# Kernel tuning notes

Hardware: AMD Instinct MI355X
Metric: run time of the kernel (lower is better)

The kernel has to match this reference:

```python
import jax, jax.numpy as jnp
import numpy as np

NUM_USERS = 4096
NUM_ITEMS = 4096
NUM_CLASSES = 5
INPUT_DIM = 64
H0 = 64   # hidden[0]
H1 = 32   # hidden[1]
BU = 2048
BV = 2048


def setup_inputs() -> dict:
    key = jax.random.key(0)
    ks = jax.random.split(key, 9)
    ridx = jax.random.randint(ks[0], (NUM_USERS, NUM_ITEMS), 0, NUM_CLASSES * 10)
    ratings = (jnp.arange(NUM_CLASSES)[:, None, None] == ridx[None]).astype(jnp.float32)
    u = jax.random.randint(ks[1], (BU,), 0, NUM_USERS)
    v = jax.random.randint(ks[2], (BV,), 0, NUM_ITEMS)
    u_emb = jax.random.normal(ks[3], (NUM_USERS, INPUT_DIM), jnp.float32) * 0.1
    v_emb = jax.random.normal(ks[4], (NUM_ITEMS, INPUT_DIM), jnp.float32) * 0.1
    gc_w = jax.random.normal(ks[5], (NUM_CLASSES, INPUT_DIM, H0), jnp.float32) / np.sqrt(INPUT_DIM)
    gc_b = jnp.zeros((NUM_CLASSES, H0), jnp.float32)
    dense_w = jax.random.normal(ks[6], (H0, H1), jnp.float32) / np.sqrt(H0)
    dense_b = jnp.zeros((H1,), jnp.float32)
    dec_w = jax.random.normal(ks[7], (NUM_CLASSES, H1, H1), jnp.float32) / np.sqrt(H1)
    return dict(u=u, v=v, ratings=ratings, u_emb=u_emb, v_emb=v_emb,
                gc_w=gc_w, gc_b=gc_b, dense_w=dense_w, dense_b=dense_b, dec_w=dec_w)


def reference(u, v, ratings, u_emb, v_emb, gc_w, gc_b, dense_w, dense_b, dec_w):
    bu = u.shape[0]
    # m = index_select(index_select(ratings, 1, u), 2, v)  -> [C, bu, bv]
    m = ratings[:, u][:, :, v]
    ue = u_emb[u]                      # [bu, D]
    ve = v_emb[v]                      # [bv, D]
    # Degree normalization exactly as in the torch code:
    # du = |sum over dim1 then dim0| -> per-item counts [bv]; di -> per-user counts [bu]
    du = jnp.abs(jnp.sum(m, axis=(0, 1)))
    di = jnp.abs(jnp.sum(m, axis=(0, 2)))
    c = jnp.concatenate([du, di])      # [bv + bu] (requires bu == bv, as in original)
    c = jnp.where(c > 0, 1.0 / c, 0.0)
    x = jnp.concatenate([ue, ve], axis=0)              # [bu+bv, D]
    # Per-class graph convolution, summed over rating classes.
    support = jnp.einsum('nd,cdh->cnh', x, gc_w)       # [C, N, H0]
    su, sv = support[:, :bu], support[:, bu:]
    agg_u = jnp.einsum('cuv,cvh->cuh', m, sv)          # users aggregate items
    agg_v = jnp.einsum('cuv,cuh->cvh', m, su)          # items aggregate users
    agg = jnp.concatenate([agg_u, agg_v], axis=1)      # [C, N, H0]
    z = jnp.sum(c[None, :, None] * agg + gc_b[:, None, :], axis=0)
    z = jax.nn.relu(z)
    hidden = jax.nn.sigmoid(z @ dense_w + dense_b)     # [N, H1]
    hu, hv = hidden[:bu], hidden[bu:]
    # Bilinear decoder: per-class logits u^T W_c v  -> [C, bu, bv]
    logits = jnp.einsum('ud,cde,ve->cuv', hu, dec_w, hv)
    probs = jax.nn.softmax(logits, axis=0)
    classes = jnp.arange(NUM_CLASSES, dtype=hidden.dtype)
    m_hat = jnp.einsum('c,cuv->uv', classes, probs)    # expected rating
    observed = jnp.sum(m, axis=0)                      # [bu, bv] in {0,1}
    n_obs = jnp.maximum(jnp.sum(observed), 1.0)
    logp = jax.nn.log_softmax(logits, axis=0)
    loss = -jnp.sum(m * logp) / n_obs
    pred = jnp.argmax(logits, axis=0)
    true = jnp.argmax(m, axis=0)
    accuracy = jnp.sum((pred == true) * observed) / n_obs
    return m_hat, loss, accuracy
```

## Files before the change

### kernel.cpp

```cpp
#include <hip/hip_runtime.h>
#include <hip/hip_bf16.h>
#include <cstdint>

#define RST 16777216
typedef unsigned short u16;
typedef unsigned char u8;
typedef __attribute__((ext_vector_type(8))) short short8v;
typedef __attribute__((ext_vector_type(4))) float f32x4;

__device__ __forceinline__ u16 f2bf(float x){
  unsigned int b = __float_as_uint(x);
  unsigned int r = (b + 0x7FFFu + ((b >> 16) & 1u)) >> 16;
  return (u16)r;
}
__device__ __forceinline__ float bf2f(u16 h){
  return __uint_as_float(((unsigned int)h) << 16);
}
__device__ __forceinline__ void split8(const float* fa, short8v& hi, short8v& lo){
#pragma unroll
  for (int e = 0; e < 8; e++){
    u16 h = f2bf(fa[e]);
    hi[e] = (short)h;
    lo[e] = (short)f2bf(fa[e] - bf2f(h));
  }
}

__global__ __launch_bounds__(256) void k_labels(const int* __restrict__ u, const int* __restrict__ v,
                                                const float* __restrict__ ratings, u8* __restrict__ L,
                                                int* __restrict__ di){
  __shared__ float row[4096];
  __shared__ int wsum[4];
  int i = blockIdx.x;
  int tid = threadIdx.x;
  int lane = tid & 63, wid = tid >> 6;
  int U = u[i];
  int j0 = tid * 8;
  int vj[8];
#pragma unroll
  for (int k = 0; k < 8; k++) vj[k] = v[j0 + k];
  int lab[8];
#pragma unroll
  for (int k = 0; k < 8; k++) lab[k] = 5;
  const float* rbase = ratings + (size_t)U * 4096;
  for (int c = 0; c < 5; c++){
    const float4* src = (const float4*)(rbase + (size_t)c * RST);
#pragma unroll
    for (int k = 0; k < 4; k++) ((float4*)row)[tid + k*256] = src[tid + k*256];
    __syncthreads();
#pragma unroll
    for (int k = 0; k < 8; k++) if (row[vj[k]] > 0.5f) lab[k] = c;
    __syncthreads();
  }
  unsigned int lo = 0, hi = 0;
  int cnt = 0;
#pragma unroll
  for (int k = 0; k < 4; k++){
    lo |= ((unsigned)lab[k]) << (8*k); hi |= ((unsigned)lab[k+4]) << (8*k);
    cnt += (lab[k] != 5); cnt += (lab[k+4] != 5);
  }
  *(uint2*)(L + (size_t)i * 2048 + j0) = make_uint2(lo, hi);
#pragma unroll
  for (int o = 32; o > 0; o >>= 1) cnt += __shfl_down(cnt, o);
  if (lane == 0) wsum[wid] = cnt;
  __syncthreads();
  if (tid == 0) di[i] = wsum[0] + wsum[1] + wsum[2] + wsum[3];
}

__global__ __launch_bounds__(256) void k_trsup(const u8* __restrict__ L, u8* __restrict__ LT,
    const int* __restrict__ u, const int* __restrict__ v,
    const float* __restrict__ u_emb, const float* __restrict__ v_emb, const float* __restrict__ gc_w,
    float* __restrict__ S){
  __shared__ u8 tile[64][64];
  int tid = threadIdx.x;
  if (blockIdx.x < 1024){
    int jb = blockIdx.x & 31, ib = blockIdx.x >> 5;
    int i0 = ib * 64, j0 = jb * 64;
    int r = tid >> 2, cq = tid & 3;
    uint4 d = *(const uint4*)(L + (size_t)(i0 + r) * 2048 + j0 + cq * 16);
    *(uint4*)&tile[r][cq * 16] = d;
    __syncthreads();
    u8 ob[16];
#pragma unroll
    for (int k = 0; k < 16; k++) ob[k] = tile[cq * 16 + k][r];
    *(uint4*)(LT + (size_t)(j0 + r) * 2048 + i0 + cq * 16) = *(uint4*)ob;
  } else {
    int b = blockIdx.x - 1024;
    int c = b >> 6, nblk = b & 63;
    int lane = tid & 63, wv = tid >> 6;
    int m = lane & 15, q = lane >> 4;
    int n0 = nblk * 64;
    bool uside = (n0 < 2048);
    const int* nidx = uside ? u : v;
    const float* emb = uside ? u_emb : v_emb;
    int nbase = uside ? n0 : (n0 - 2048);
    int h0 = wv * 16;
    short8v bh[2], bl[2];
#pragma unroll
    for (int ch = 0; ch < 2; ch++){
      const float* wp = gc_w + c * 4096 + (ch * 32 + q * 8) * 64 + h0 + m;
      float fb[8];
#pragma unroll
      for (int e = 0; e < 8; e++) fb[e] = wp[e * 64];
      split8(fb, bh[ch], bl[ch]);
    }
#pragma unroll
    for (int rt = 0; rt < 4; rt++){
      const float* xr = emb + (size_t)nidx[nbase + rt * 16 + m] * 64;
      f32x4 acc = {0.f, 0.f, 0.f, 0.f};
#pragma unroll
      for (int ch = 0; ch < 2; ch++){
        float fa[8];
        *(float4*)&fa[0] = *(const float4*)(xr + ch * 32 + q * 8);
        *(float4*)&fa[4] = *(const float4*)(xr + ch * 32 + q * 8 + 4);
        short8v ah, al;
        split8(fa, ah, al);
        acc = __builtin_amdgcn_mfma_f32_16x16x32_bf16(ah, bh[ch], acc, 0, 0, 0);
        acc = __builtin_amdgcn_mfma_f32_16x16x32_bf16(ah, bl[ch], acc, 0, 0, 0);
        acc = __builtin_amdgcn_mfma_f32_16x16x32_bf16(al, bh[ch], acc, 0, 0, 0);
      }
      int h = h0 + m;
      int rbase = n0 + rt * 16 + q * 4;
#pragma unroll
      for (int reg = 0; reg < 4; reg++)
        S[((size_t)c * 4096 + rbase + reg) * 64 + h] = acc[reg];
    }
  }
}

__global__ __launch_bounds__(256) void k_agg(const u8* __restrict__ L, const u8* __restrict__ LT,
    const float* __restrict__ S, float* __restrict__ aggsum, int* __restrict__ du){
  __shared__ u16 lst[2048];
  __shared__ int wbase[4];
  __shared__ float red[4][64];
  int r = blockIdx.x;
  int tid = threadIdx.x;
  int lane = tid & 63, wid = tid >> 6;
  bool uside = (r < 2048);
  const u8* rowp = uside ? (L + (size_t)r * 2048) : (LT + (size_t)(r - 2048) * 2048);
  uint2 d = ((const uint2*)rowp)[tid];
  int lab[8];
#pragma unroll
  for (int k = 0; k < 4; k++){ lab[k] = (d.x >> (8*k)) & 255; lab[k+4] = (d.y >> (8*k)) & 255; }
  int cnt = 0;
#pragma unroll
  for (int k = 0; k < 8; k++) cnt += (lab[k] != 5);
  int pre = cnt;
#pragma unroll
  for (int o = 1; o < 64; o <<= 1){ int t = __shfl_up(pre, o); if (lane >= o) pre += t; }
  if (lane == 63) wbase[wid] = pre;
  __syncthreads();
  int base = 0;
#pragma unroll
  for (int w = 0; w < 4; w++) base += (w < wid) ? wbase[w] : 0;
  int total = wbase[0] + wbase[1] + wbase[2] + wbase[3];
  int off = base + (pre - cnt);
  int j0 = tid * 8;
#pragma unroll
  for (int k = 0; k < 8; k++)
    if (lab[k] != 5) lst[off++] = (u16)(((j0 + k) << 3) | lab[k]);
  if (!uside && tid == 0) du[r - 2048] = total;
  __syncthreads();
  const float* Sop = S + (uside ? 131072 : 0) + lane;
  int e0 = (wid * total) >> 2, e1 = ((wid + 1) * total) >> 2;
  float a0 = 0.f, a1 = 0.f, a2 = 0.f, a3 = 0.f;
  int e = e0;
  for (; e + 4 <= e1; e += 4){
    int x0 = lst[e], x1 = lst[e+1], x2 = lst[e+2], x3 = lst[e+3];
    a0 += Sop[(size_t)(x0 & 7) * 262144 + (size_t)(x0 >> 3) * 64];
    a1 += Sop[(size_t)(x1 & 7) * 262144 + (size_t)(x1 >> 3) * 64];
    a2 += Sop[(size_t)(x2 & 7) * 262144 + (size_t)(x2 >> 3) * 64];
    a3 += Sop[(size_t)(x3 & 7) * 262144 + (size_t)(x3 >> 3) * 64];
  }
  for (; e < e1; e++){
    int x = lst[e];
    a0 += Sop[(size_t)(x & 7) * 262144 + (size_t)(x >> 3) * 64];
  }
  red[wid][lane] = (a0 + a1) + (a2 + a3);
  __syncthreads();
  if (wid == 0) aggsum[(size_t)r * 64 + lane] = red[0][lane] + red[1][lane] + red[2][lane] + red[3][lane];
}

__global__ __launch_bounds__(256) void k_hidden(const float* __restrict__ aggsum, const int* __restrict__ du, const int* __restrict__ di,
    const float* __restrict__ gc_b, const float* __restrict__ dense_w, const float* __restrict__ dense_b,
    float* __restrict__ hidden){
  int wid = threadIdx.x >> 6, lane = threadIdx.x & 63;
  int r = blockIdx.x * 4 + wid;
  float a = aggsum[(size_t)r * 64 + lane];
  int cnt = (r < 2048) ? du[r] : di[r - 2048];
  float inv = (cnt > 0) ? (1.0f / (float)cnt) : 0.0f;
  float bsum = 0.f;
#pragma unroll
  for (int c = 0; c < 5; c++) bsum += gc_b[c * 64 + lane];
  float z = fmaxf(a * inv + bsum, 0.f);
  __shared__ float zb[4][64];
  zb[wid][lane] = z;
  __syncthreads();
  if (lane < 32){
    float s = dense_b[lane];
#pragma unroll
    for (int h = 0; h < 64; h++) s += zb[wid][h] * dense_w[h * 32 + lane];
    hidden[(size_t)r * 32 + lane] = 1.0f / (1.0f + __expf(-s));
  }
}

#define EPI(l, lab, outp) do{ \
  float mx = fmaxf(fmaxf(fmaxf(l[0], l[1]), fmaxf(l[2], l[3])), l[4]); \
  float e0 = __expf(l[0]-mx), e1 = __expf(l[1]-mx), e2 = __expf(l[2]-mx), e3 = __expf(l[3]-mx), e4 = __expf(l[4]-mx); \
  float ssum = e0 + e1 + e2 + e3 + e4; \
  *(outp) = (e1 + 2.f*e2 + 3.f*e3 + 4.f*e4) / ssum; \
  if ((lab) < 5){ \
    int pred = 0; float bm = l[0]; \
    if (l[1] > bm){ bm = l[1]; pred = 1; } \
    if (l[2] > bm){ bm = l[2]; pred = 2; } \
    if (l[3] > bm){ bm = l[3]; pred = 3; } \
    if (l[4] > bm){ bm = l[4]; pred = 4; } \
    float ll = (lab)==0 ? l[0] : ((lab)==1 ? l[1] : ((lab)==2 ? l[2] : ((lab)==3 ? l[3] : l[4]))); \
    lsum += __logf(ssum) + mx - ll; \
    acnt += (pred == (lab)); \
  } \
}while(0)

__global__ __launch_bounds__(256) void k_logits(const float* __restrict__ hidden, const float* __restrict__ dec_w,
    const u8* __restrict__ L, float* __restrict__ mhat, float* __restrict__ lpart, int* __restrict__ apart){
  __shared__ float hu_s[512];
  __shared__ float tsf[5 * 16 * 36];
  int tid = threadIdx.x;
  int lane = tid & 63, w = tid >> 6;
  int i0 = blockIdx.y * 16;
  if (tid < 128) ((float4*)hu_s)[tid] = ((const float4*)(hidden + (size_t)i0 * 32))[tid];
  __syncthreads();
  for (int idx = tid; idx < 2560; idx += 256){
    int c = idx >> 9; int rem = idx & 511; int ii = rem >> 5; int e = rem & 31;
    const float* wc = dec_w + (size_t)c * 1024 + e;
    const float* hr = hu_s + ii * 32;
    float s = 0.f;
#pragma unroll
    for (int d = 0; d < 32; d++) s += hr[d] * wc[d * 32];
    tsf[(c * 16 + ii) * 36 + e] = s;
  }
  __syncthreads();
  int m = lane & 15, q = lane >> 4;
  short8v a_hi[5], a_lo[5];
#pragma unroll
  for (int c = 0; c < 5; c++){
    const float* p = &tsf[(c * 16 + m) * 36 + q * 8];
    float fa[8];
    *(float4*)&fa[0] = *(const float4*)p;
    *(float4*)&fa[4] = *(const float4*)(p + 4);
    split8(fa, a_hi[c], a_lo[c]);
  }
  const float* hv = hidden + 2048 * 32;
  float lsum = 0.f; int acnt = 0;
  int jw0 = blockIdx.x * 256 + w * 64;
#pragma unroll
  for (int jj = 0; jj < 4; jj++){
    int j0 = jw0 + jj * 16;
    const float* pb = hv + (size_t)(j0 + m) * 32 + q * 8;
    float fb[8];
    *(float4*)&fb[0] = *(const float4*)pb;
    *(float4*)&fb[4] = *(const float4*)(pb + 4);
    short8v b_hi, b_lo;
    split8(fb, b_hi, b_lo);
    f32x4 acc[5];
    f32x4 z4 = {0.f, 0.f, 0.f, 0.f};
#pragma unroll
    for (int c = 0; c < 5; c++){
      f32x4 a = __builtin_amdgcn_mfma_f32_16x16x32_bf16(a_hi[c], b_hi, z4, 0, 0, 0);
      a = __builtin_amdgcn_mfma_f32_16x16x32_bf16(a_hi[c], b_lo, a, 0, 0, 0);
      a = __builtin_amdgcn_mfma_f32_16x16x32_bf16(a_lo[c], b_hi, a, 0, 0, 0);
      acc[c] = a;
    }
    int jcol = j0 + m;
#pragma unroll
    for (int r = 0; r < 4; r++){
      int irow = i0 + q * 4 + r;
      float l5[5] = {acc[0][r], acc[1][r], acc[2][r], acc[3][r], acc[4][r]};
      int lab = L[(size_t)irow * 2048 + jcol];
      EPI(l5, lab, mhat + (size_t)irow * 2048 + jcol);
    }
  }
#pragma unroll
  for (int o = 32; o > 0; o >>= 1){ lsum += __shfl_down(lsum, o); acnt += __shfl_down(acnt, o); }
  __shared__ float wl[4]; __shared__ int wa[4];
  if (lane == 0){ wl[w] = lsum; wa[w] = acnt; }
  __syncthreads();
  if (tid == 0){
    int pb = blockIdx.y * 8 + blockIdx.x;
    lpart[pb] = wl[0] + wl[1] + wl[2] + wl[3];
    apart[pb] = wa[0] + wa[1] + wa[2] + wa[3];
  }
}

__global__ __launch_bounds__(256) void k_final(const float* __restrict__ lpart, const int* __restrict__ apart,
                                               const int* __restrict__ di, float* __restrict__ out){
  __shared__ float lred[256];
  __shared__ int ared[256], nred[256];
  int tid = threadIdx.x;
  float ls = 0.f; int as = 0;
#pragma unroll
  for (int k = 0; k < 4; k++){ ls += lpart[tid + k * 256]; as += apart[tid + k * 256]; }
  int ns = 0;
#pragma unroll
  for (int k = 0; k < 8; k++) ns += di[tid + k * 256];
  lred[tid] = ls; ared[tid] = as; nred[tid] = ns;
  __syncthreads();
  for (int s = 128; s > 0; s >>= 1){
    if (tid < s){ lred[tid] += lred[tid + s]; ared[tid] += ared[tid + s]; nred[tid] += nred[tid + s]; }
    __syncthreads();
  }
  if (tid == 0){
    float n = fmaxf((float)nred[0], 1.0f);
    out[0] = lred[0] / n;
    out[1] = ((float)ared[0]) / n;
  }
}

extern "C" void kernel_launch(void* const* d_in, const int* in_sizes, int n_in,
                              void* d_out, int out_size, void* d_ws, size_t ws_size,
                              hipStream_t stream){
  const int*   u       = (const int*)d_in[0];
  const int*   v       = (const int*)d_in[1];
  const float* ratings = (const float*)d_in[2];
  const float* u_emb   = (const float*)d_in[3];
  const float* v_emb   = (const float*)d_in[4];
  const float* gc_w    = (const float*)d_in[5];
  const float* gc_b    = (const float*)d_in[6];
  const float* dense_w = (const float*)d_in[7];
  const float* dense_b = (const float*)d_in[8];
  const float* dec_w   = (const float*)d_in[9];
  float* out = (float*)d_out;
  char* ws = (char*)d_ws;

  u8*    L       = (u8*)(ws + 0);
  u8*    LT      = (u8*)(ws + 4194304);
  float* S       = (float*)(ws + 8388608);
  float* aggsum  = (float*)(ws + 13631488);
  float* hidden  = (float*)(ws + 14680064);
  int*   du      = (int*)(ws + 15204352);
  int*   di      = (int*)(ws + 15212544);
  float* lpart   = (float*)(ws + 15220736);
  int*   apart   = (int*)(ws + 15224832);

  k_labels <<<2048, 256, 0, stream>>>(u, v, ratings, L, di);
  k_trsup  <<<1344, 256, 0, stream>>>(L, LT, u, v, u_emb, v_emb, gc_w, S);
  k_agg    <<<4096, 256, 0, stream>>>(L, LT, S, aggsum, du);
  k_hidden <<<1024, 256, 0, stream>>>(aggsum, du, di, gc_b, dense_w, dense_b, hidden);
  k_logits <<<dim3(8, 128), 256, 0, stream>>>(hidden, dec_w, L, out, lpart, apart);
  k_final  <<<1, 256, 0, stream>>>(lpart, apart, di, out + 4194304);
}
```

Measured before the change: 94.03 us.

## Replace sparse gather aggregation with dense one-hot MFMA matmul over label matrix

The per-row sparse list build and scattered gathers in the aggregation kernel are replaced by a dense matmul: one-hot masks built from the byte label matrix are multiplied against support stored as transposed hi/lo bf16 pairs using MFMA, split over 16 K-chunks. Partial results go to a larger workspace and are summed in the hidden kernel, which now also recomputes the item degree counts from LT. This trades irregular gathers for regular but ~10x denser tensor-core work, extra partial-sum traffic, and 2-term bf16 split precision.

New measurement: 104.4 us. 11.0% more time.

```diff
diff --git a/kernel.cpp b/kernel.cpp
--- a/kernel.cpp
+++ b/kernel.cpp
@@ -5,6 +5,7 @@
 #define RST 16777216
 typedef unsigned short u16;
 typedef unsigned char u8;
+typedef unsigned int u32;
 typedef __attribute__((ext_vector_type(8))) short short8v;
 typedef __attribute__((ext_vector_type(4))) float f32x4;
 
@@ -23,6 +24,12 @@
     hi[e] = (short)h;
     lo[e] = (short)f2bf(fa[e] - bf2f(h));
   }
+}
+__device__ __forceinline__ int cnt_not5(u32 w){
+  int c = 0;
+  c += ((w & 255u) != 5u); c += (((w >> 8) & 255u) != 5u);
+  c += (((w >> 16) & 255u) != 5u); c += ((w >> 24) != 5u);
+  return c;
 }
 
 __global__ __launch_bounds__(256) void k_labels(const int* __restrict__ u, const int* __restrict__ v,
@@ -69,7 +76,7 @@
 __global__ __launch_bounds__(256) void k_trsup(const u8* __restrict__ L, u8* __restrict__ LT,
     const int* __restrict__ u, const int* __restrict__ v,
     const float* __restrict__ u_emb, const float* __restrict__ v_emb, const float* __restrict__ gc_w,
-    float* __restrict__ S){
+    u32* __restrict__ SP){
   __shared__ u8 tile[64][64];
   int tid = threadIdx.x;
   if (blockIdx.x < 1024){
@@ -121,72 +128,91 @@
       int h = h0 + m;
       int rbase = n0 + rt * 16 + q * 4;
 #pragma unroll
-      for (int reg = 0; reg < 4; reg++)
-        S[((size_t)c * 4096 + rbase + reg) * 64 + h] = acc[reg];
+      for (int reg = 0; reg < 4; reg++){
+        float val = acc[reg];
+        u16 vh = f2bf(val);
+        u16 vl = f2bf(val - bf2f(vh));
+        SP[(((size_t)c * 64 + h) << 12) + rbase + reg] = (((u32)vh) << 16) | (u32)vl;
+      }
     }
   }
 }
 
 __global__ __launch_bounds__(256) void k_agg(const u8* __restrict__ L, const u8* __restrict__ LT,
-    const float* __restrict__ S, float* __restrict__ aggsum, int* __restrict__ du){
-  __shared__ u16 lst[2048];
-  __shared__ int wbase[4];
-  __shared__ float red[4][64];
-  int r = blockIdx.x;
-  int tid = threadIdx.x;
-  int lane = tid & 63, wid = tid >> 6;
-  bool uside = (r < 2048);
-  const u8* rowp = uside ? (L + (size_t)r * 2048) : (LT + (size_t)(r - 2048) * 2048);
-  uint2 d = ((const uint2*)rowp)[tid];
-  int lab[8];
-#pragma unroll
-  for (int k = 0; k < 4; k++){ lab[k] = (d.x >> (8*k)) & 255; lab[k+4] = (d.y >> (8*k)) & 255; }
-  int cnt = 0;
-#pragma unroll
-  for (int k = 0; k < 8; k++) cnt += (lab[k] != 5);
-  int pre = cnt;
-#pragma unroll
-  for (int o = 1; o < 64; o <<= 1){ int t = __shfl_up(pre, o); if (lane >= o) pre += t; }
-  if (lane == 63) wbase[wid] = pre;
-  __syncthreads();
-  int base = 0;
-#pragma unroll
-  for (int w = 0; w < 4; w++) base += (w < wid) ? wbase[w] : 0;
-  int total = wbase[0] + wbase[1] + wbase[2] + wbase[3];
-  int off = base + (pre - cnt);
-  int j0 = tid * 8;
-#pragma unroll
-  for (int k = 0; k < 8; k++)
-    if (lab[k] != 5) lst[off++] = (u16)(((j0 + k) << 3) | lab[k]);
-  if (!uside && tid == 0) du[r - 2048] = total;
-  __syncthreads();
-  const float* Sop = S + (uside ? 131072 : 0) + lane;
-  int e0 = (wid * total) >> 2, e1 = ((wid + 1) * total) >> 2;
-  float a0 = 0.f, a1 = 0.f, a2 = 0.f, a3 = 0.f;
-  int e = e0;
-  for (; e + 4 <= e1; e += 4){
-    int x0 = lst[e], x1 = lst[e+1], x2 = lst[e+2], x3 = lst[e+3];
-    a0 += Sop[(size_t)(x0 & 7) * 262144 + (size_t)(x0 >> 3) * 64];
-    a1 += Sop[(size_t)(x1 & 7) * 262144 + (size_t)(x1 >> 3) * 64];
-    a2 += Sop[(size_t)(x2 & 7) * 262144 + (size_t)(x2 >> 3) * 64];
-    a3 += Sop[(size_t)(x3 & 7) * 262144 + (size_t)(x3 >> 3) * 64];
-  }
-  for (; e < e1; e++){
-    int x = lst[e];
-    a0 += Sop[(size_t)(x & 7) * 262144 + (size_t)(x >> 3) * 64];
-  }
-  red[wid][lane] = (a0 + a1) + (a2 + a3);
-  __syncthreads();
-  if (wid == 0) aggsum[(size_t)r * 64 + lane] = red[0][lane] + red[1][lane] + red[2][lane] + red[3][lane];
-}
-
-__global__ __launch_bounds__(256) void k_hidden(const float* __restrict__ aggsum, const int* __restrict__ du, const int* __restrict__ di,
+    const u32* __restrict__ SP, float* __restrict__ aggp){
+  int tid = threadIdx.x;
+  int lane = tid & 63, wv = tid >> 6;
+  int m = lane & 15, q = lane >> 4;
+  int kc = blockIdx.x;
+  int rb = blockIdx.y;
+  int r0 = rb * 64;
+  bool uside = (r0 < 2048);
+  const u8* Ab = uside ? (L + (size_t)r0 * 2048) : (LT + (size_t)(r0 - 2048) * 2048);
+  int nb = uside ? 2048 : 0;
+  int h0 = wv * 16;
+  f32x4 acc[4];
+#pragma unroll
+  for (int it = 0; it < 4; it++) acc[it] = (f32x4){0.f, 0.f, 0.f, 0.f};
+  for (int ks = 0; ks < 4; ks++){
+    int j0 = (kc * 4 + ks) * 32;
+    short8v bh[5], bl[5];
+#pragma unroll
+    for (int c = 0; c < 5; c++){
+      const uint4* bp = (const uint4*)(SP + (((size_t)c * 64 + h0 + m) << 12) + nb + j0 + q * 8);
+      uint4 wA = bp[0], wB = bp[1];
+      u32 wws[8] = {wA.x, wA.y, wA.z, wA.w, wB.x, wB.y, wB.z, wB.w};
+#pragma unroll
+      for (int e = 0; e < 8; e++){
+        bh[c][e] = (short)(wws[e] >> 16);
+        bl[c][e] = (short)(wws[e] & 0xffffu);
+      }
+    }
+#pragma unroll
+    for (int it = 0; it < 4; it++){
+      uint2 aw = *(const uint2*)(Ab + (size_t)(it * 16 + m) * 2048 + j0 + q * 8);
+      int b[8];
+#pragma unroll
+      for (int e = 0; e < 4; e++){ b[e] = (aw.x >> (8*e)) & 255; b[e+4] = (aw.y >> (8*e)) & 255; }
+#pragma unroll
+      for (int c = 0; c < 5; c++){
+        short8v am;
+#pragma unroll
+        for (int e = 0; e < 8; e++) am[e] = (short)((b[e] == c) ? 0x3F80 : 0);
+        acc[it] = __builtin_amdgcn_mfma_f32_16x16x32_bf16(am, bh[c], acc[it], 0, 0, 0);
+        acc[it] = __builtin_amdgcn_mfma_f32_16x16x32_bf16(am, bl[c], acc[it], 0, 0, 0);
+      }
+    }
+  }
+  float* op = aggp + (size_t)kc * 262144;
+#pragma unroll
+  for (int it = 0; it < 4; it++){
+#pragma unroll
+    for (int reg = 0; reg < 4; reg++)
+      op[(size_t)(r0 + it * 16 + q * 4 + reg) * 64 + h0 + m] = acc[it][reg];
+  }
+}
+
+__global__ __launch_bounds__(256) void k_hidden(const float* __restrict__ aggp, const u8* __restrict__ LT,
+    const int* __restrict__ di,
     const float* __restrict__ gc_b, const float* __restrict__ dense_w, const float* __restrict__ dense_b,
     float* __restrict__ hidden){
   int wid = threadIdx.x >> 6, lane = threadIdx.x & 63;
   int r = blockIdx.x * 4 + wid;
-  float a = aggsum[(size_t)r * 64 + lane];
-  int cnt = (r < 2048) ? du[r] : di[r - 2048];
+  float a = 0.f;
+#pragma unroll
+  for (int kc = 0; kc < 16; kc++) a += aggp[(size_t)kc * 262144 + (size_t)r * 64 + lane];
+  int cnt;
+  if (r < 2048){
+    const uint4* rp = (const uint4*)(LT + (size_t)r * 2048);
+    uint4 w1 = rp[lane * 2], w2 = rp[lane * 2 + 1];
+    int c2 = cnt_not5(w1.x) + cnt_not5(w1.y) + cnt_not5(w1.z) + cnt_not5(w1.w)
+           + cnt_not5(w2.x) + cnt_not5(w2.y) + cnt_not5(w2.z) + cnt_not5(w2.w);
+#pragma unroll
+    for (int o = 32; o > 0; o >>= 1) c2 += __shfl_down(c2, o);
+    cnt = __shfl(c2, 0);
+  } else {
+    cnt = di[r - 2048];
+  }
   float inv = (cnt > 0) ? (1.0f / (float)cnt) : 0.0f;
   float bsum = 0.f;
 #pragma unroll
@@ -333,18 +359,17 @@
 
   u8*    L       = (u8*)(ws + 0);
   u8*    LT      = (u8*)(ws + 4194304);
-  float* S       = (float*)(ws + 8388608);
-  float* aggsum  = (float*)(ws + 13631488);
-  float* hidden  = (float*)(ws + 14680064);
-  int*   du      = (int*)(ws + 15204352);
-  int*   di      = (int*)(ws + 15212544);
-  float* lpart   = (float*)(ws + 15220736);
-  int*   apart   = (int*)(ws + 15224832);
+  u32*   SP      = (u32*)(ws + 8388608);
+  float* aggp    = (float*)(ws + 13631488);
+  float* hidden  = (float*)(ws + 30408704);
+  int*   di      = (int*)(ws + 30932992);
+  float* lpart   = (float*)(ws + 30941184);
+  int*   apart   = (int*)(ws + 30945280);
 
   k_labels <<<2048, 256, 0, stream>>>(u, v, ratings, L, di);
-  k_trsup  <<<1344, 256, 0, stream>>>(L, LT, u, v, u_emb, v_emb, gc_w, S);
-  k_agg    <<<4096, 256, 0, stream>>>(L, LT, S, aggsum, du);
-  k_hidden <<<1024, 256, 0, stream>>>(aggsum, du, di, gc_b, dense_w, dense_b, hidden);
+  k_trsup  <<<1344, 256, 0, stream>>>(L, LT, u, v, u_emb, v_emb, gc_w, SP);
+  k_agg    <<<dim3(16, 64), 256, 0, stream>>>(L, LT, SP, aggp);
+  k_hidden <<<1024, 256, 0, stream>>>(aggp, LT, di, gc_b, dense_w, dense_b, hidden);
   k_logits <<<dim3(8, 128), 256, 0, stream>>>(hidden, dec_w, L, out, lpart, apart);
   k_final  <<<1, 256, 0, stream>>>(lpart, apart, di, out + 4194304);
 }
```
